# Kernel tuning notes

Measured on AMD Instinct MI355X. Metric: run time of the kernel, lower is better.

## Reference

```python
import jax, jax.numpy as jnp
import numpy as np

N = 20000
E = 320000
DIN = 256
DH = 64
DOUT = 64
H = 8
NEG_SLOPE = 0.2


def _glorot(key, shape):
    fan_in, fan_out = shape[0], shape[-1]
    lim = jnp.sqrt(6.0 / (fan_in + fan_out))
    return jax.random.uniform(key, shape, jnp.float32, -lim, lim)


def setup_inputs() -> dict:
    key = jax.random.key(0)
    ks = jax.random.split(key, 12)
    x = jax.random.normal(ks[0], (N, DIN), jnp.float32)
    edge_index = jax.random.randint(ks[1], (2, E), 0, N, jnp.int32)
    # layer 1: dim_in -> heads*dim_h
    Wl1 = _glorot(ks[2], (DIN, H * DH));  bl1 = jnp.zeros((H * DH,), jnp.float32)
    Wr1 = _glorot(ks[3], (DIN, H * DH));  br1 = jnp.zeros((H * DH,), jnp.float32)
    att1 = _glorot(ks[4], (H, DH))
    bias1 = jnp.zeros((H * DH,), jnp.float32)
    # layer 2: heads*dim_h -> heads*dim_out
    Wl2 = _glorot(ks[5], (H * DH, H * DOUT)); bl2 = jnp.zeros((H * DOUT,), jnp.float32)
    Wr2 = _glorot(ks[6], (H * DH, H * DOUT)); br2 = jnp.zeros((H * DOUT,), jnp.float32)
    att2 = _glorot(ks[7], (H, DOUT))
    bias2 = jnp.zeros((H * DOUT,), jnp.float32)
    return dict(x=x, edge_index=edge_index, Wl1=Wl1, bl1=bl1, Wr1=Wr1, br1=br1,
                att1=att1, bias1=bias1, Wl2=Wl2, bl2=bl2, Wr2=Wr2, br2=br2,
                att2=att2, bias2=bias2)


def _gatv2(x, src, dst, Wl, bl, Wr, br, att, bias_out, heads, out_ch):
    n = x.shape[0]
    l = (x @ Wl + bl).reshape(n, heads, out_ch)   # source transform
    r = (x @ Wr + br).reshape(n, heads, out_ch)   # target transform
    # per-edge GATv2 score: att . LeakyReLU(l_j + r_i)
    e = jax.nn.leaky_relu(l[src] + r[dst], NEG_SLOPE)      # [E, H, C]
    logits = jnp.einsum('ehc,hc->eh', e, att)              # [E, H]
    # segmented softmax over incoming edges of each destination node
    m = jax.ops.segment_max(logits, dst, num_segments=n)   # [N, H]
    expd = jnp.exp(logits - m[dst])
    denom = jax.ops.segment_sum(expd, dst, num_segments=n)
    alpha = expd / denom[dst]                              # [E, H]
    msg = l[src] * alpha[:, :, None]                       # [E, H, C]
    out = jax.ops.segment_sum(msg, dst, num_segments=n)    # [N, H, C]
    return out.reshape(n, heads * out_ch) + bias_out


def reference(x, edge_index, Wl1, bl1, Wr1, br1, att1, bias1,
              Wl2, bl2, Wr2, br2, att2, bias2):
    n = x.shape[0]
    loops = jnp.arange(n, dtype=edge_index.dtype)
    src = jnp.concatenate([edge_index[0], loops])  # GATv2Conv adds self-loops
    dst = jnp.concatenate([edge_index[1], loops])
    # dropout is identity at inference
    h = _gatv2(x, src, dst, Wl1, bl1, Wr1, br1, att1, bias1, H, DH)
    h = jax.nn.elu(h)
    h = _gatv2(h, src, dst, Wl2, bl2, Wr2, br2, att2, bias2, H, DOUT)
    return h, jax.nn.log_softmax(h, axis=1)
```

## Files before the change

### kernel.cpp

```cpp
#include <hip/hip_runtime.h>
#include <math.h>

#define NN   20000
#define NE   320000
#define ET   (NE + NN)
#define CPAD 16
#define D_IN 256
#define DHID 512
#define NLR  1024
#define MPAD 20096

typedef __attribute__((ext_vector_type(8))) short bf16x8;
typedef __attribute__((ext_vector_type(4))) float f32x4;

typedef __attribute__((address_space(3))) uint       lds_uint;
typedef __attribute__((address_space(1))) const uint gbl_uint;
#define ASYNC16(gp, lp) \
    __builtin_amdgcn_global_load_lds((gbl_uint*)(gp), (lds_uint*)(lp), 16, 0, 0)

__device__ __forceinline__ ushort f2bf(float f) {
    uint u = __float_as_uint(f);
    return (ushort)((u + 0x7fffu + ((u >> 16) & 1u)) >> 16);
}


__global__ __launch_bounds__(256) void init_count(int* count, int* csr_src) {
    int i = blockIdx.x * 256 + threadIdx.x;
    if (i < NN) count[i] = 1;
    if (i < CPAD) csr_src[ET + i] = 0;
}

__global__ __launch_bounds__(256) void hist_kernel(const int* __restrict__ dstv,
                                                   int* __restrict__ count) {
    int e = blockIdx.x * 256 + threadIdx.x;
    if (e < NE) atomicAdd(&count[dstv[e]], 1);
}

__global__ __launch_bounds__(1024) void scan_kernel(const int* __restrict__ count,
                                                    int* __restrict__ offs,
                                                    int* __restrict__ cursor) {
    __shared__ int sm[1024];
    const int CH = 20;
    int t = threadIdx.x;
    int base = t * CH;
    int local[CH];
    int s = 0;
#pragma unroll
    for (int i = 0; i < CH; i++) {
        int idx = base + i;
        int v = (idx < NN) ? count[idx] : 0;
        local[i] = s;
        s += v;
    }
    sm[t] = s;
    __syncthreads();
    for (int o = 1; o < 1024; o <<= 1) {
        int v = (t >= o) ? sm[t - o] : 0;
        __syncthreads();
        sm[t] += v;
        __syncthreads();
    }
    int pref = (t > 0) ? sm[t - 1] : 0;
#pragma unroll
    for (int i = 0; i < CH; i++) {
        int idx = base + i;
        if (idx < NN) {
            int o_ = pref + local[i];
            offs[idx] = o_;
            cursor[idx] = o_;
        }
    }
    if (t == 1023) offs[NN] = sm[1023];
}

__global__ __launch_bounds__(256) void scatter_kernel(const int* __restrict__ srcv,
                                                      const int* __restrict__ dstv,
                                                      int* __restrict__ cursor,
                                                      int* __restrict__ csr_src) {
    int e = blockIdx.x * 256 + threadIdx.x;
    if (e >= ET) return;
    int s, d;
    if (e < NE) { s = srcv[e]; d = dstv[e]; }
    else        { s = e - NE;  d = s; }
    int pos = atomicAdd(&cursor[d], 1);
    csr_src[pos] = s;
}


__global__ __launch_bounds__(256) void convert_x(const float* __restrict__ x,
                                                 ushort* __restrict__ a) {
    long e = ((long)blockIdx.x * 256 + threadIdx.x) * 4;
    if (e >= (long)MPAD * D_IN) return;
    int row = (int)(e >> 8);
    float4 v = make_float4(0.f, 0.f, 0.f, 0.f);
    if (row < NN) v = *(const float4*)&x[e];
    ushort4 o;
    o.x = f2bf(v.x); o.y = f2bf(v.y); o.z = f2bf(v.z); o.w = f2bf(v.w);
    *(ushort4*)&a[e] = o;
}

__global__ __launch_bounds__(256) void zero_pad2(ushort* __restrict__ a) {
    int t = blockIdx.x * 256 + threadIdx.x;
    if (t < (MPAD - NN) * DHID / 4) {
        ushort4 z = {0, 0, 0, 0};
        *(ushort4*)&a[(long)NN * DHID + (long)t * 4] = z;
    }
}

__global__ __launch_bounds__(256) void transpose_w(const float* __restrict__ Wl,
                                                   const float* __restrict__ Wr,
                                                   ushort* __restrict__ Wt, int K) {
    __shared__ float tile[32][33];
    int k0 = blockIdx.x * 32, n0 = blockIdx.y * 32;
    int tx = threadIdx.x & 31, ty = threadIdx.x >> 5;
    const float* __restrict__ W = (n0 < DHID) ? Wl : Wr;
    int nb = (n0 < DHID) ? n0 : n0 - DHID;
#pragma unroll
    for (int r = ty; r < 32; r += 8)
        tile[r][tx] = W[(long)(k0 + r) * DHID + nb + tx];
    __syncthreads();
#pragma unroll
    for (int r = ty; r < 32; r += 8)
        Wt[(long)(n0 + r) * K + k0 + tx] = f2bf(tile[tx][r]);
}


#define BM 128
#define BN 128
#define BK 64

__global__ __launch_bounds__(256) void gemm_mfma(const ushort* __restrict__ A, int K,
                                                 const ushort* __restrict__ Wt,
                                                 const float* __restrict__ bl,
                                                 const float* __restrict__ br,
                                                 ushort* __restrict__ out) {
    __shared__ ushort As[BM * BK];
    __shared__ ushort Bs[BN * BK];

    int t = threadIdx.x;
    int row0 = blockIdx.x * BM;
    int col0 = blockIdx.y * BN;

    int lane = t & 63, w = t >> 6;
    int wr = w >> 1, wc = w & 1;
    int l16 = lane & 15, lhi = lane >> 4;

    f32x4 acc[4][4];
#pragma unroll
    for (int m = 0; m < 4; m++)
#pragma unroll
        for (int n = 0; n < 4; n++)
            acc[m][n] = (f32x4){0.f, 0.f, 0.f, 0.f};

    for (int k0 = 0; k0 < K; k0 += BK) {
#pragma unroll
        for (int q = 0; q < 4; q++) {
            int chunk = q * 256 + t;
            int row = chunk >> 3;
            int il = (chunk & 7) ^ (row & 7);
            ASYNC16(A  + (long)(row0 + row) * K + k0 + il * 8, (char*)As + chunk * 16);
            ASYNC16(Wt + (long)(col0 + row) * K + k0 + il * 8, (char*)Bs + chunk * 16);
        }
        __syncthreads();
#pragma unroll
        for (int kk = 0; kk < 2; kk++) {
            bf16x8 af[4], bfr[4];
#pragma unroll
            for (int m = 0; m < 4; m++) {
                int rl = wr * 64 + m * 16 + l16;
                int off = rl * 128 + ((kk * 64 + lhi * 16) ^ ((rl & 7) << 4));
                af[m] = *(const bf16x8*)((const char*)As + off);
            }
#pragma unroll
            for (int n = 0; n < 4; n++) {
                int rl = wc * 64 + n * 16 + l16;
                int off = rl * 128 + ((kk * 64 + lhi * 16) ^ ((rl & 7) << 4));
                bfr[n] = *(const bf16x8*)((const char*)Bs + off);
            }
#pragma unroll
            for (int m = 0; m < 4; m++)
#pragma unroll
                for (int n = 0; n < 4; n++)
                    acc[m][n] = __builtin_amdgcn_mfma_f32_16x16x32_bf16(af[m], bfr[n], acc[m][n], 0, 0, 0);
        }
        __syncthreads();
    }

    float bvn[4];
#pragma unroll
    for (int n = 0; n < 4; n++) {
        int col = col0 + wc * 64 + n * 16 + l16;
        bvn[n] = (col < DHID) ? bl[col] : br[col - DHID];
    }
#pragma unroll
    for (int m = 0; m < 4; m++) {
        int rbase = row0 + wr * 64 + m * 16 + lhi * 4;
#pragma unroll
        for (int j = 0; j < 4; j++) {
            int row = rbase + j;
            if (row < NN) {
#pragma unroll
                for (int n = 0; n < 4; n++) {
                    int col = col0 + wc * 64 + n * 16 + l16;
                    out[(long)row * NLR + col] = f2bf(acc[m][n][j] + bvn[n]);
                }
            }
        }
    }
}


#define CVT8(u, f)                                  \
    f[0] = __uint_as_float((u).x << 16);            \
    f[1] = __uint_as_float((u).x & 0xffff0000u);    \
    f[2] = __uint_as_float((u).y << 16);            \
    f[3] = __uint_as_float((u).y & 0xffff0000u);    \
    f[4] = __uint_as_float((u).z << 16);            \
    f[5] = __uint_as_float((u).z & 0xffff0000u);    \
    f[6] = __uint_as_float((u).w << 16);            \
    f[7] = __uint_as_float((u).w & 0xffff0000u);

template <int MODE>
__global__ __launch_bounds__(256) void aggregate_kernel(const ushort* __restrict__ lr,
                                                        const float* __restrict__ att,
                                                        const float* __restrict__ bias,
                                                        const int* __restrict__ csr_src,
                                                        const int* __restrict__ offs,
                                                        ushort* __restrict__ out_bf,
                                                        float* __restrict__ out_f32,
                                                        float* __restrict__ out_lsm) {
    int i = blockIdx.x * 4 + (threadIdx.x >> 6);
    int lane = threadIdx.x & 63;
    int c0 = lane << 3;

    uint4 ur = *(const uint4*)(lr + (long)i * NLR + DHID + c0);
    float rv[8];
    CVT8(ur, rv);
    float a06[8], a04[8];
    float4 at0 = *(const float4*)&att[c0];
    float4 at1 = *(const float4*)&att[c0 + 4];
    const float K06 = 0.6f * 1.44269504f, K04 = 0.4f * 1.44269504f;
    a06[0] = at0.x * K06; a06[1] = at0.y * K06; a06[2] = at0.z * K06; a06[3] = at0.w * K06;
    a06[4] = at1.x * K06; a06[5] = at1.y * K06; a06[6] = at1.z * K06; a06[7] = at1.w * K06;
    a04[0] = at0.x * K04; a04[1] = at0.y * K04; a04[2] = at0.z * K04; a04[3] = at0.w * K04;
    a04[4] = at1.x * K04; a04[5] = at1.y * K04; a04[6] = at1.z * K04; a04[7] = at1.w * K04;

    int beg = offs[i], end = offs[i + 1];
    float m = -3.0e38f, d = 0.f;
    float acc[8] = {0.f, 0.f, 0.f, 0.f, 0.f, 0.f, 0.f, 0.f};

    int j = csr_src[beg];
    uint4 v = *(const uint4*)(lr + (long)j * NLR + c0);

    for (int k = beg; k < end; k++) {
        uint4 vc = v;
        int jn = csr_src[k + 1];
        v = *(const uint4*)(lr + (long)jn * NLR + c0);

        float lx[8];
        CVT8(vc, lx);
        float s = 0.f;
#pragma unroll
        for (int c = 0; c < 8; c++) {
            float tt = lx[c] + rv[c];
            s = fmaf(a06[c], tt, s);
            s = fmaf(a04[c], __builtin_fabsf(tt), s);
        }
        s += __shfl_xor(s, 1);
        s += __shfl_xor(s, 2);
        s += __shfl_xor(s, 4);

        if (s > m) {
            float sc = exp2f(m - s);
            d *= sc;
#pragma unroll
            for (int c = 0; c < 8; c++) acc[c] *= sc;
            m = s;
        }
        float wgt = exp2f(s - m);
        d += wgt;
#pragma unroll
        for (int c = 0; c < 8; c++) acc[c] = fmaf(wgt, lx[c], acc[c]);
    }

    float inv = 1.f / d;
    float o[8];
    float4 bi0 = *(const float4*)&bias[c0];
    float4 bi1 = *(const float4*)&bias[c0 + 4];
    o[0] = fmaf(acc[0], inv, bi0.x); o[1] = fmaf(acc[1], inv, bi0.y);
    o[2] = fmaf(acc[2], inv, bi0.z); o[3] = fmaf(acc[3], inv, bi0.w);
    o[4] = fmaf(acc[4], inv, bi1.x); o[5] = fmaf(acc[5], inv, bi1.y);
    o[6] = fmaf(acc[6], inv, bi1.z); o[7] = fmaf(acc[7], inv, bi1.w);

    if (MODE == 0) {
#pragma unroll
        for (int c = 0; c < 8; c++) o[c] = (o[c] > 0.f) ? o[c] : expm1f(o[c]);
        uint4 p;
        p.x = (uint)f2bf(o[0]) | ((uint)f2bf(o[1]) << 16);
        p.y = (uint)f2bf(o[2]) | ((uint)f2bf(o[3]) << 16);
        p.z = (uint)f2bf(o[4]) | ((uint)f2bf(o[5]) << 16);
        p.w = (uint)f2bf(o[6]) | ((uint)f2bf(o[7]) << 16);
        *(uint4*)(out_bf + (long)i * DHID + c0) = p;
    } else {
        *(float4*)&out_f32[(long)i * DHID + c0]     = *(float4*)&o[0];
        *(float4*)&out_f32[(long)i * DHID + c0 + 4] = *(float4*)&o[4];
        float mx = o[0];
#pragma unroll
        for (int c = 1; c < 8; c++) mx = fmaxf(mx, o[c]);
#pragma unroll
        for (int off = 1; off < 64; off <<= 1) mx = fmaxf(mx, __shfl_xor(mx, off));
        float se = 0.f;
#pragma unroll
        for (int c = 0; c < 8; c++) se += __expf(o[c] - mx);
#pragma unroll
        for (int off = 1; off < 64; off <<= 1) se += __shfl_xor(se, off);
        float lg = mx + logf(se);
        float l0[8];
#pragma unroll
        for (int c = 0; c < 8; c++) l0[c] = o[c] - lg;
        *(float4*)&out_lsm[(long)i * DHID + c0]     = *(float4*)&l0[0];
        *(float4*)&out_lsm[(long)i * DHID + c0 + 4] = *(float4*)&l0[4];
    }
}


extern "C" void kernel_launch(void* const* d_in, const int* in_sizes, int n_in,
                              void* d_out, int out_size, void* d_ws, size_t ws_size,
                              hipStream_t stream) {
    const float* x     = (const float*)d_in[0];
    const int*   ei    = (const int*)d_in[1];
    const float* Wl1   = (const float*)d_in[2];
    const float* bl1   = (const float*)d_in[3];
    const float* Wr1   = (const float*)d_in[4];
    const float* br1   = (const float*)d_in[5];
    const float* att1  = (const float*)d_in[6];
    const float* bias1 = (const float*)d_in[7];
    const float* Wl2   = (const float*)d_in[8];
    const float* bl2   = (const float*)d_in[9];
    const float* Wr2   = (const float*)d_in[10];
    const float* br2   = (const float*)d_in[11];
    const float* att2  = (const float*)d_in[12];
    const float* bias2 = (const float*)d_in[13];

    float* out = (float*)d_out;
    float* h2  = out;
    float* lsm = out + (long)NN * DHID;

    ushort* lrbuf  = (ushort*)d_ws;
    ushort* Abf    = lrbuf + (long)NN * NLR;
    ushort* Wt1    = Abf + (long)MPAD * DHID;
    ushort* Wt2    = Wt1 + (long)NLR * D_IN;
    int*    csr_src = (int*)(Wt2 + (long)NLR * DHID);
    int*    count   = csr_src + ET + CPAD;
    int*    offs    = count + NN;
    int*    cursor  = offs + NN + 1;

    const int* srcv = ei;
    const int* dstv = ei + NE;

    convert_x<<<(MPAD * D_IN / 4 + 255) / 256, 256, 0, stream>>>(x, Abf);
    zero_pad2<<<((MPAD - NN) * DHID / 4 + 255) / 256, 256, 0, stream>>>(Abf);
    transpose_w<<<dim3(D_IN / 32, NLR / 32), 256, 0, stream>>>(Wl1, Wr1, Wt1, D_IN);
    transpose_w<<<dim3(DHID / 32, NLR / 32), 256, 0, stream>>>(Wl2, Wr2, Wt2, DHID);

    init_count<<<(NN + 255) / 256, 256, 0, stream>>>(count, csr_src);
    hist_kernel<<<(NE + 255) / 256, 256, 0, stream>>>(dstv, count);
    scan_kernel<<<1, 1024, 0, stream>>>(count, offs, cursor);
    scatter_kernel<<<(ET + 255) / 256, 256, 0, stream>>>(srcv, dstv, cursor, csr_src);

    dim3 ggrid((NN + BM - 1) / BM, NLR / BN);

    gemm_mfma<<<ggrid, 256, 0, stream>>>(Abf, D_IN, Wt1, bl1, br1, lrbuf);
    aggregate_kernel<0><<<NN / 4, 256, 0, stream>>>(lrbuf, att1, bias1, csr_src, offs, Abf, nullptr, nullptr);

    gemm_mfma<<<ggrid, 256, 0, stream>>>(Abf, DHID, Wt2, bl2, br2, lrbuf);
    aggregate_kernel<1><<<NN / 4, 256, 0, stream>>>(lrbuf, att2, bias2, csr_src, offs, nullptr, h2, lsm);
}
```

Before: 263.2 us.

## Merge prep kernels, vectorize GEMM epilogue stores, simplify edge score math

```diff
diff --git a/kernel.cpp b/kernel.cpp
--- a/kernel.cpp
+++ b/kernel.cpp
@@ -87,33 +87,43 @@
 }
 
 
-__global__ __launch_bounds__(256) void convert_x(const float* __restrict__ x,
-                                                 ushort* __restrict__ a) {
-    long e = ((long)blockIdx.x * 256 + threadIdx.x) * 4;
-    if (e >= (long)MPAD * D_IN) return;
-    int row = (int)(e >> 8);
-    float4 v = make_float4(0.f, 0.f, 0.f, 0.f);
-    if (row < NN) v = *(const float4*)&x[e];
-    ushort4 o;
-    o.x = f2bf(v.x); o.y = f2bf(v.y); o.z = f2bf(v.z); o.w = f2bf(v.w);
-    *(ushort4*)&a[e] = o;
-}
-
-__global__ __launch_bounds__(256) void zero_pad2(ushort* __restrict__ a) {
-    int t = blockIdx.x * 256 + threadIdx.x;
-    if (t < (MPAD - NN) * DHID / 4) {
+#define N1Q ((long)MPAD * D_IN / 4)
+#define N2Q ((long)(MPAD - NN) * DHID / 4)
+
+__global__ __launch_bounds__(256) void prep_a(const float* __restrict__ x,
+                                              ushort* __restrict__ a) {
+    long t = (long)blockIdx.x * 256 + threadIdx.x;
+    if (t < N1Q) {
+        long e = t * 4;
+        int row = (int)(e >> 8);
+        float4 v = make_float4(0.f, 0.f, 0.f, 0.f);
+        if (row < NN) v = *(const float4*)&x[e];
+        ushort4 o;
+        o.x = f2bf(v.x); o.y = f2bf(v.y); o.z = f2bf(v.z); o.w = f2bf(v.w);
+        *(ushort4*)&a[e] = o;
+    } else if (t < N1Q + N2Q) {
+        long e = (t - N1Q) * 4 + (long)NN * DHID;
         ushort4 z = {0, 0, 0, 0};
-        *(ushort4*)&a[(long)NN * DHID + (long)t * 4] = z;
-    }
-}
-
-__global__ __launch_bounds__(256) void transpose_w(const float* __restrict__ Wl,
-                                                   const float* __restrict__ Wr,
-                                                   ushort* __restrict__ Wt, int K) {
+        *(ushort4*)&a[e] = z;
+    }
+}
+
+
+__global__ __launch_bounds__(256) void transpose_w2(const float* __restrict__ Wl1,
+                                                    const float* __restrict__ Wr1,
+                                                    ushort* __restrict__ Wt1,
+                                                    const float* __restrict__ Wl2,
+                                                    const float* __restrict__ Wr2,
+                                                    ushort* __restrict__ Wt2) {
     __shared__ float tile[32][33];
-    int k0 = blockIdx.x * 32, n0 = blockIdx.y * 32;
+    int z = blockIdx.z;
+    int K = z ? DHID : D_IN;
+    int k0 = blockIdx.x * 32;
+    if (k0 >= K) return;
+    int n0 = blockIdx.y * 32;
     int tx = threadIdx.x & 31, ty = threadIdx.x >> 5;
-    const float* __restrict__ W = (n0 < DHID) ? Wl : Wr;
+    const float* __restrict__ W = (n0 < DHID) ? (z ? Wl2 : Wl1) : (z ? Wr2 : Wr1);
+    ushort* __restrict__ Wt = z ? Wt2 : Wt1;
     int nb = (n0 < DHID) ? n0 : n0 - DHID;
 #pragma unroll
     for (int r = ty; r < 32; r += 8)
@@ -181,29 +191,31 @@
             for (int m = 0; m < 4; m++)
 #pragma unroll
                 for (int n = 0; n < 4; n++)
-                    acc[m][n] = __builtin_amdgcn_mfma_f32_16x16x32_bf16(af[m], bfr[n], acc[m][n], 0, 0, 0);
+                    acc[m][n] = __builtin_amdgcn_mfma_f32_16x16x32_bf16(bfr[n], af[m], acc[m][n], 0, 0, 0);
         }
         __syncthreads();
     }
 
-    float bvn[4];
+    float4 bvn[4];
 #pragma unroll
     for (int n = 0; n < 4; n++) {
-        int col = col0 + wc * 64 + n * 16 + l16;
-        bvn[n] = (col < DHID) ? bl[col] : br[col - DHID];
+        int colb = col0 + wc * 64 + n * 16 + lhi * 4;
+        bvn[n] = (colb < DHID) ? *(const float4*)&bl[colb]
+                               : *(const float4*)&br[colb - DHID];
     }
 #pragma unroll
     for (int m = 0; m < 4; m++) {
-        int rbase = row0 + wr * 64 + m * 16 + lhi * 4;
-#pragma unroll
-        for (int j = 0; j < 4; j++) {
-            int row = rbase + j;
-            if (row < NN) {
-#pragma unroll
-                for (int n = 0; n < 4; n++) {
-                    int col = col0 + wc * 64 + n * 16 + l16;
-                    out[(long)row * NLR + col] = f2bf(acc[m][n][j] + bvn[n]);
-                }
+        int row = row0 + wr * 64 + m * 16 + l16;
+        if (row < NN) {
+#pragma unroll
+            for (int n = 0; n < 4; n++) {
+                int colb = col0 + wc * 64 + n * 16 + lhi * 4;
+                ushort4 p;
+                p.x = f2bf(acc[m][n][0] + bvn[n].x);
+                p.y = f2bf(acc[m][n][1] + bvn[n].y);
+                p.z = f2bf(acc[m][n][2] + bvn[n].z);
+                p.w = f2bf(acc[m][n][3] + bvn[n].w);
+                *(ushort4*)&out[(long)row * NLR + colb] = p;
             }
         }
     }
@@ -236,14 +248,9 @@
     uint4 ur = *(const uint4*)(lr + (long)i * NLR + DHID + c0);
     float rv[8];
     CVT8(ur, rv);
-    float a06[8], a04[8];
-    float4 at0 = *(const float4*)&att[c0];
-    float4 at1 = *(const float4*)&att[c0 + 4];
-    const float K06 = 0.6f * 1.44269504f, K04 = 0.4f * 1.44269504f;
-    a06[0] = at0.x * K06; a06[1] = at0.y * K06; a06[2] = at0.z * K06; a06[3] = at0.w * K06;
-    a06[4] = at1.x * K06; a06[5] = at1.y * K06; a06[6] = at1.z * K06; a06[7] = at1.w * K06;
-    a04[0] = at0.x * K04; a04[1] = at0.y * K04; a04[2] = at0.z * K04; a04[3] = at0.w * K04;
-    a04[4] = at1.x * K04; a04[5] = at1.y * K04; a04[6] = at1.z * K04; a04[7] = at1.w * K04;
+    float av[8];
+    *(float4*)&av[0] = *(const float4*)&att[c0];
+    *(float4*)&av[4] = *(const float4*)&att[c0 + 4];
 
     int beg = offs[i], end = offs[i + 1];
     float m = -3.0e38f, d = 0.f;
@@ -254,7 +261,8 @@
 
     for (int k = beg; k < end; k++) {
         uint4 vc = v;
-        int jn = csr_src[k + 1];
+        int kn = (k + 1 < end) ? k + 1 : k;
+        int jn = csr_src[kn];
         v = *(const uint4*)(lr + (long)jn * NLR + c0);
 
         float lx[8];
@@ -262,10 +270,11 @@
         float s = 0.f;
 #pragma unroll
         for (int c = 0; c < 8; c++) {
-            float tt = lx[c] + rv[c];
-            s = fmaf(a06[c], tt, s);
-            s = fmaf(a04[c], __builtin_fabsf(tt), s);
-        }
+            float e = lx[c] + rv[c];
+            e = fmaxf(e, 0.2f * e);
+            s = fmaf(av[c], e, s);
+        }
+        s *= 1.44269504f;
         s += __shfl_xor(s, 1);
         s += __shfl_xor(s, 2);
         s += __shfl_xor(s, 4);
@@ -358,10 +367,9 @@
     const int* srcv = ei;
     const int* dstv = ei + NE;
 
-    convert_x<<<(MPAD * D_IN / 4 + 255) / 256, 256, 0, stream>>>(x, Abf);
-    zero_pad2<<<((MPAD - NN) * DHID / 4 + 255) / 256, 256, 0, stream>>>(Abf);
-    transpose_w<<<dim3(D_IN / 32, NLR / 32), 256, 0, stream>>>(Wl1, Wr1, Wt1, D_IN);
-    transpose_w<<<dim3(DHID / 32, NLR / 32), 256, 0, stream>>>(Wl2, Wr2, Wt2, DHID);
+    prep_a<<<(int)((N1Q + N2Q + 255) / 256), 256, 0, stream>>>(x, Abf);
+    transpose_w2<<<dim3(DHID / 32, NLR / 32, 2), 256, 0, stream>>>(Wl1, Wr1, Wt1,
+                                                                   Wl2, Wr2, Wt2);
 
     init_count<<<(NN + 255) / 256, 256, 0, stream>>>(count, csr_src);
     hist_kernel<<<(NE + 255) / 256, 256, 0, stream>>>(dstv, count);
```

Result: slower. 269.3 us (+2.3%).
